# Kernel tuning notes

Measured on AMD Instinct MI355X. Metric: run time of the kernel, lower is better.

Reference implementation:

```python
import jax, jax.numpy as jnp
import numpy as np


def setup_inputs() -> dict:
    key = jax.random.key(0)
    k = jax.random.split(key, 8)
    B, S, D, H = 4, 4096, 1024, 4096
    x = jax.random.normal(k[0], (B, S, D), dtype=jnp.float32)
    # per-output-channel symmetric int8 weights in [-127, 127]
    w1_q = jax.random.randint(k[1], (H, D), -127, 128, dtype=jnp.int32)
    w2_q = jax.random.randint(k[2], (D, H), -127, 128, dtype=jnp.int32)
    # positive per-channel scales, roughly max|W|/127 for W ~ N(0, 0.02)
    s1 = jax.random.uniform(k[3], (H,), dtype=jnp.float32, minval=0.5, maxval=1.5) * (0.02 / 127.0)
    s2 = jax.random.uniform(k[4], (D,), dtype=jnp.float32, minval=0.5, maxval=1.5) * (0.02 / 127.0)
    b1 = jax.random.normal(k[5], (H,), dtype=jnp.float32) * 0.01
    b2 = jax.random.normal(k[6], (D,), dtype=jnp.float32) * 0.01
    return {"x": x, "w1_q": w1_q, "s1": s1, "b1": b1, "w2_q": w2_q, "s2": s2, "b2": b2}


def reference(x, w1_q, s1, b1, w2_q, s2, b2):
    # fc1: dequantize per-output-channel int8 weights, then GEMM + bias
    w1 = w1_q.astype(jnp.float32) * s1[:, None]          # [H, D]
    h = jnp.einsum('bsd,hd->bsh', x, w1) + b1            # [B, S, H]
    h = jax.nn.gelu(h, approximate=False)                # exact erf GELU (torch F.gelu default)
    # fc2: dequant + GEMM + bias
    w2 = w2_q.astype(jnp.float32) * s2[:, None]          # [D, H]
    y = jnp.einsum('bsh,dh->bsd', h, w2) + b2            # [B, S, D]
    return y
```

## Files before the change

kernel.cpp:

```cpp
#include <hip/hip_runtime.h>
#include <hip/hip_bf16.h>
#include <math.h>


typedef short bf16x8 __attribute__((ext_vector_type(8)));
typedef float f32x4 __attribute__((ext_vector_type(4)));

__device__ __forceinline__ unsigned short f2bf(float f) {
  unsigned int x = __float_as_uint(f);
  unsigned int r = (x + 0x7FFFu + ((x >> 16) & 1u)) >> 16;
  return (unsigned short)r;
}


__global__ void cvt_f32_bf16(const float* __restrict__ in,
                             unsigned short* __restrict__ out, int n4) {
  int i = blockIdx.x * blockDim.x + threadIdx.x;
  if (i >= n4) return;
  float4 v = reinterpret_cast<const float4*>(in)[i];
  ushort4 o;
  o.x = f2bf(v.x); o.y = f2bf(v.y); o.z = f2bf(v.z); o.w = f2bf(v.w);
  reinterpret_cast<ushort4*>(out)[i] = o;
}

__global__ void cvt_i32_bf16(const int* __restrict__ in,
                             unsigned short* __restrict__ out, int n4) {
  int i = blockIdx.x * blockDim.x + threadIdx.x;
  if (i >= n4) return;
  int4 v = reinterpret_cast<const int4*>(in)[i];
  ushort4 o;
  o.x = f2bf((float)v.x); o.y = f2bf((float)v.y);
  o.z = f2bf((float)v.z); o.w = f2bf((float)v.w);
  reinterpret_cast<ushort4*>(out)[i] = o;
}


#define BM 128
#define BN 128
#define BK 64

template <int EPI>
__global__ __launch_bounds__(256, 2) void gemm_bt(
    const unsigned short* __restrict__ A, const unsigned short* __restrict__ Bw,
    const float* __restrict__ scale, const float* __restrict__ bias,
    void* __restrict__ Cout, int M, int N, int K) {
  __shared__ unsigned short As[BM * BK];
  __shared__ unsigned short Bs[BN * BK];

  const int nwg = gridDim.x;
  const int orig = blockIdx.x;
  const int q = nwg >> 3, r = nwg & 7;
  const int xcd = orig & 7, idx = orig >> 3;
  const int swz =
      (xcd < r ? xcd * (q + 1) : r * (q + 1) + (xcd - r) * q) + idx;

  const int nBn = N / BN;
  const int bm = (swz / nBn) * BM;
  const int bn = (swz % nBn) * BN;

  const int tid = threadIdx.x;
  const int lane = tid & 63;
  const int wid = tid >> 6;
  const int wm = (wid >> 1) * 64;
  const int wn = (wid & 1) * 64;

  const int r0 = tid >> 3;
  const int c0 = (tid & 7) * 8;

  const unsigned short* aSrc = A + (size_t)(bm + r0) * K + c0;
  const unsigned short* bSrc = Bw + (size_t)(bn + r0) * K + c0;
  unsigned short* aDst = &As[r0 * BK + c0];
  unsigned short* bDst = &Bs[r0 * BK + c0];

  f32x4 acc[4][4];
#pragma unroll
  for (int i = 0; i < 4; ++i)
#pragma unroll
    for (int j = 0; j < 4; ++j) acc[i][j] = 0.0f;

  const int kIters = K / BK;
  for (int ks = 0; ks < kIters; ++ks) {
    const unsigned short* aS = aSrc + ks * BK;
    const unsigned short* bS = bSrc + ks * BK;
#pragma unroll
    for (int i = 0; i < 4; ++i) {
      __builtin_amdgcn_global_load_lds(
          (const __attribute__((address_space(1))) void*)(aS + (size_t)i * 32 * K),
          (__attribute__((address_space(3))) void*)(aDst + i * 32 * BK), 16, 0, 0);
    }
#pragma unroll
    for (int i = 0; i < 4; ++i) {
      __builtin_amdgcn_global_load_lds(
          (const __attribute__((address_space(1))) void*)(bS + (size_t)i * 32 * K),
          (__attribute__((address_space(3))) void*)(bDst + i * 32 * BK), 16, 0, 0);
    }
    __syncthreads();

#pragma unroll
    for (int kk = 0; kk < BK; kk += 32) {
      const int kOff = kk + (lane >> 4) * 8;
      bf16x8 a[4], b[4];
#pragma unroll
      for (int mi = 0; mi < 4; ++mi)
        a[mi] = *(const bf16x8*)&As[(wm + mi * 16 + (lane & 15)) * BK + kOff];
#pragma unroll
      for (int ni = 0; ni < 4; ++ni)
        b[ni] = *(const bf16x8*)&Bs[(wn + ni * 16 + (lane & 15)) * BK + kOff];
#pragma unroll
      for (int mi = 0; mi < 4; ++mi)
#pragma unroll
        for (int ni = 0; ni < 4; ++ni)
          acc[mi][ni] = __builtin_amdgcn_mfma_f32_16x16x32_bf16(
              a[mi], b[ni], acc[mi][ni], 0, 0, 0);
    }
    __syncthreads();
  }

  const int cr = (lane >> 4) * 4;
  const int cc = lane & 15;
#pragma unroll
  for (int ni = 0; ni < 4; ++ni) {
    const int gn = bn + wn + ni * 16 + cc;
    const float sv = scale[gn];
    const float bv = bias[gn];
#pragma unroll
    for (int mi = 0; mi < 4; ++mi) {
#pragma unroll
      for (int qq = 0; qq < 4; ++qq) {
        const size_t gm = (size_t)(bm + wm + mi * 16 + cr + qq);
        float v = acc[mi][ni][qq] * sv + bv;
        if (EPI == 0) {
          v = 0.5f * v * (1.0f + erff(v * 0.70710678118654752f));
          ((unsigned short*)Cout)[gm * N + gn] = f2bf(v);
        } else {
          ((float*)Cout)[gm * N + gn] = v;
        }
      }
    }
  }
}


extern "C" void kernel_launch(void* const* d_in, const int* in_sizes, int n_in,
                              void* d_out, int out_size, void* d_ws,
                              size_t ws_size, hipStream_t stream) {
  const float* x = (const float*)d_in[0];
  const int* w1q = (const int*)d_in[1];
  const float* s1 = (const float*)d_in[2];
  const float* b1 = (const float*)d_in[3];
  const int* w2q = (const int*)d_in[4];
  const float* s2 = (const float*)d_in[5];
  const float* b2 = (const float*)d_in[6];

  const int H = in_sizes[3];
  const int D = in_sizes[6];
  const int M = in_sizes[0] / D;

  char* ws = (char*)d_ws;
  unsigned short* xb = (unsigned short*)ws;  ws += (size_t)M * D * 2;
  unsigned short* w1b = (unsigned short*)ws; ws += (size_t)H * D * 2;
  unsigned short* w2b = (unsigned short*)ws; ws += (size_t)D * H * 2;
  unsigned short* hb = (unsigned short*)ws;  ws += (size_t)M * H * 2;

  {
    int n4 = M * D / 4;
    cvt_f32_bf16<<<(n4 + 255) / 256, 256, 0, stream>>>(x, xb, n4);
  }
  {
    int n4 = H * D / 4;
    cvt_i32_bf16<<<(n4 + 255) / 256, 256, 0, stream>>>(w1q, w1b, n4);
    cvt_i32_bf16<<<(n4 + 255) / 256, 256, 0, stream>>>(w2q, w2b, n4);
  }

  gemm_bt<0><<<(M / BM) * (H / BN), 256, 0, stream>>>(
      xb, w1b, s1, b1, (void*)hb, M, H, D);
  gemm_bt<1><<<(M / BM) * (D / BN), 256, 0, stream>>>(
      hb, w2b, s2, b2, d_out, M, D, H);
}
```

Before: 492.1 us.

## Rewrite GEMM as 256x256 tile, 8-wave, software-pipelined kernel with swizzled LDS

Replaces the 128x128 single-buffer GEMM with a 512-thread kernel that computes 256x256 output tiles. The K dimension is split into 32-wide slices staged into double-buffered LDS slots via global_load_lds, with a four-phase schedule that interleaves next-slice loads with MFMA work, raised priority around the MFMAs, and an XOR swizzle to avoid LDS bank conflicts. Conversion kernels now use grid-stride loops with 8-element vectors. This aims to overlap memory with compute and raise reuse per tile. In exchange, register pressure is higher with 32 accumulators per thread, and correctness depends on the hand-placed barriers and waitcnts.

```diff
diff --git a/kernel.cpp b/kernel.cpp
--- a/kernel.cpp
+++ b/kernel.cpp
@@ -5,6 +5,7 @@
 
 typedef short bf16x8 __attribute__((ext_vector_type(8)));
 typedef float f32x4 __attribute__((ext_vector_type(4)));
+typedef unsigned short u16x8 __attribute__((ext_vector_type(8)));
 
 __device__ __forceinline__ unsigned short f2bf(float f) {
   unsigned int x = __float_as_uint(f);
@@ -14,121 +15,170 @@
 
 
 __global__ void cvt_f32_bf16(const float* __restrict__ in,
-                             unsigned short* __restrict__ out, int n4) {
-  int i = blockIdx.x * blockDim.x + threadIdx.x;
-  if (i >= n4) return;
-  float4 v = reinterpret_cast<const float4*>(in)[i];
-  ushort4 o;
-  o.x = f2bf(v.x); o.y = f2bf(v.y); o.z = f2bf(v.z); o.w = f2bf(v.w);
-  reinterpret_cast<ushort4*>(out)[i] = o;
+                             unsigned short* __restrict__ out, int n8) {
+  const int stride = gridDim.x * blockDim.x;
+  for (int i = blockIdx.x * blockDim.x + threadIdx.x; i < n8; i += stride) {
+    const float4* p = (const float4*)(in + (size_t)i * 8);
+    float4 v0 = p[0], v1 = p[1];
+    u16x8 o;
+    o[0] = f2bf(v0.x); o[1] = f2bf(v0.y); o[2] = f2bf(v0.z); o[3] = f2bf(v0.w);
+    o[4] = f2bf(v1.x); o[5] = f2bf(v1.y); o[6] = f2bf(v1.z); o[7] = f2bf(v1.w);
+    *(u16x8*)(out + (size_t)i * 8) = o;
+  }
 }
 
 __global__ void cvt_i32_bf16(const int* __restrict__ in,
-                             unsigned short* __restrict__ out, int n4) {
-  int i = blockIdx.x * blockDim.x + threadIdx.x;
-  if (i >= n4) return;
-  int4 v = reinterpret_cast<const int4*>(in)[i];
-  ushort4 o;
-  o.x = f2bf((float)v.x); o.y = f2bf((float)v.y);
-  o.z = f2bf((float)v.z); o.w = f2bf((float)v.w);
-  reinterpret_cast<ushort4*>(out)[i] = o;
-}
-
-
-#define BM 128
-#define BN 128
-#define BK 64
+                             unsigned short* __restrict__ out, int n8) {
+  const int stride = gridDim.x * blockDim.x;
+  for (int i = blockIdx.x * blockDim.x + threadIdx.x; i < n8; i += stride) {
+    const int4* p = (const int4*)(in + (size_t)i * 8);
+    int4 v0 = p[0], v1 = p[1];
+    u16x8 o;
+    o[0] = f2bf((float)v0.x); o[1] = f2bf((float)v0.y);
+    o[2] = f2bf((float)v0.z); o[3] = f2bf((float)v0.w);
+    o[4] = f2bf((float)v1.x); o[5] = f2bf((float)v1.y);
+    o[6] = f2bf((float)v1.z); o[7] = f2bf((float)v1.w);
+    *(u16x8*)(out + (size_t)i * 8) = o;
+  }
+}
+
+
+#define NSLOT 8
+#define SLOTE 4096
+
+__device__ __forceinline__ void stage_half(
+    const unsigned short* __restrict__ gA, const unsigned short* __restrict__ gB,
+    int bm, int bn, int K, unsigned short* lds, int T, int w, int tid) {
+  const unsigned short* base =
+      (w >= 2) ? (gB + (size_t)(bn + (w & 1) * 128) * K)
+               : (gA + (size_t)(bm + (w & 1) * 128) * K);
+  base += T * 32;
+  unsigned short* slot = lds + ((((T & 1) << 2) | w) * SLOTE);
+  const int lr = tid >> 2;
+  const int colD = (tid & 3) * 8;
+  const int colS = colD ^ ((lr & 3) << 3);
+  __builtin_amdgcn_global_load_lds(
+      (const __attribute__((address_space(1))) void*)(base + (size_t)lr * K + colS),
+      (__attribute__((address_space(3))) void*)(slot + lr * 32 + colD), 16, 0, 0);
+}
+
+#define DS_A(asl, mi) \
+  (*(const bf16x8*)&lds[(asl) * SLOTE + ((mi) * 16 + l15) * 32 + c0])
+#define DS_B(bsl, ni) \
+  (*(const bf16x8*)&lds[(bsl) * SLOTE + (bRow + (ni) * 16 + l15) * 32 + c0])
+
+#define PHASE(p, sAslot, sBslot, STAGE, VM)                                    \
+  {                                                                            \
+    bf16x8 a0, a1;                                                             \
+    if ((p) == 0) {                                                            \
+      _Pragma("unroll") for (int ni = 0; ni < 4; ++ni) bfr[ni] =               \
+          DS_B(sBslot, ni);                                                    \
+    }                                                                          \
+    a0 = DS_A(sAslot, 2 * (p));                                                \
+    a1 = DS_A(sAslot, 2 * (p) + 1);                                            \
+    STAGE;                                                                     \
+    VM;                                                                        \
+    __builtin_amdgcn_s_barrier();                                              \
+    asm volatile("s_waitcnt lgkmcnt(0)" ::: "memory");                         \
+    __builtin_amdgcn_sched_barrier(0);                                         \
+    __builtin_amdgcn_s_setprio(1);                                             \
+    _Pragma("unroll") for (int ni = 0; ni < 4; ++ni) {                         \
+      acc[2 * (p)][ni] = __builtin_amdgcn_mfma_f32_16x16x32_bf16(              \
+          a0, bfr[ni], acc[2 * (p)][ni], 0, 0, 0);                             \
+      acc[2 * (p) + 1][ni] = __builtin_amdgcn_mfma_f32_16x16x32_bf16(          \
+          a1, bfr[ni], acc[2 * (p) + 1][ni], 0, 0, 0);                         \
+    }                                                                          \
+    __builtin_amdgcn_s_setprio(0);                                             \
+    __builtin_amdgcn_sched_barrier(0);                                         \
+    __builtin_amdgcn_s_barrier();                                              \
+  }
+
+#define VM2 asm volatile("s_waitcnt vmcnt(2)" ::: "memory")
+#define VM0 asm volatile("s_waitcnt vmcnt(0)" ::: "memory")
+#define STG(T_, w_) stage_half(A, Bw, bm, bn, K, lds, (T_), (w_), tid)
 
 template <int EPI>
-__global__ __launch_bounds__(256, 2) void gemm_bt(
+__global__ __launch_bounds__(512) void gemm8p(
     const unsigned short* __restrict__ A, const unsigned short* __restrict__ Bw,
     const float* __restrict__ scale, const float* __restrict__ bias,
     void* __restrict__ Cout, int M, int N, int K) {
-  __shared__ unsigned short As[BM * BK];
-  __shared__ unsigned short Bs[BN * BK];
+  __shared__ unsigned short lds[NSLOT * SLOTE];
 
   const int nwg = gridDim.x;
   const int orig = blockIdx.x;
-  const int q = nwg >> 3, r = nwg & 7;
-  const int xcd = orig & 7, idx = orig >> 3;
+  const int qx = nwg >> 3, rx = nwg & 7;
+  const int xcd = orig & 7, sidx = orig >> 3;
   const int swz =
-      (xcd < r ? xcd * (q + 1) : r * (q + 1) + (xcd - r) * q) + idx;
-
-  const int nBn = N / BN;
-  const int bm = (swz / nBn) * BM;
-  const int bn = (swz % nBn) * BN;
+      (xcd < rx ? xcd * (qx + 1) : rx * (qx + 1) + (xcd - rx) * qx) + sidx;
+
+  const int nBn = N / 256;
+  const int bm = (swz / nBn) * 256;
+  const int bn = (swz % nBn) * 256;
 
   const int tid = threadIdx.x;
   const int lane = tid & 63;
   const int wid = tid >> 6;
-  const int wm = (wid >> 1) * 64;
-  const int wn = (wid & 1) * 64;
-
-  const int r0 = tid >> 3;
-  const int c0 = (tid & 7) * 8;
-
-  const unsigned short* aSrc = A + (size_t)(bm + r0) * K + c0;
-  const unsigned short* bSrc = Bw + (size_t)(bn + r0) * K + c0;
-  unsigned short* aDst = &As[r0 * BK + c0];
-  unsigned short* bDst = &Bs[r0 * BK + c0];
-
-  f32x4 acc[4][4];
-#pragma unroll
-  for (int i = 0; i < 4; ++i)
+  const int wm = wid >> 2;
+  const int wn = wid & 3;
+
+  const int l15 = lane & 15;
+  const int c0 = (((lane >> 4) * 8)) ^ ((lane & 3) << 3);
+  const int bRow = (wn & 1) * 64;
+  const int bHalf = 2 + (wn >> 1);
+
+  f32x4 acc[8][4];
+#pragma unroll
+  for (int i = 0; i < 8; ++i)
 #pragma unroll
     for (int j = 0; j < 4; ++j) acc[i][j] = 0.0f;
 
-  const int kIters = K / BK;
-  for (int ks = 0; ks < kIters; ++ks) {
-    const unsigned short* aS = aSrc + ks * BK;
-    const unsigned short* bS = bSrc + ks * BK;
-#pragma unroll
-    for (int i = 0; i < 4; ++i) {
-      __builtin_amdgcn_global_load_lds(
-          (const __attribute__((address_space(1))) void*)(aS + (size_t)i * 32 * K),
-          (__attribute__((address_space(3))) void*)(aDst + i * 32 * BK), 16, 0, 0);
-    }
-#pragma unroll
-    for (int i = 0; i < 4; ++i) {
-      __builtin_amdgcn_global_load_lds(
-          (const __attribute__((address_space(1))) void*)(bS + (size_t)i * 32 * K),
-          (__attribute__((address_space(3))) void*)(bDst + i * 32 * BK), 16, 0, 0);
-    }
-    __syncthreads();
-
-#pragma unroll
-    for (int kk = 0; kk < BK; kk += 32) {
-      const int kOff = kk + (lane >> 4) * 8;
-      bf16x8 a[4], b[4];
-#pragma unroll
-      for (int mi = 0; mi < 4; ++mi)
-        a[mi] = *(const bf16x8*)&As[(wm + mi * 16 + (lane & 15)) * BK + kOff];
-#pragma unroll
-      for (int ni = 0; ni < 4; ++ni)
-        b[ni] = *(const bf16x8*)&Bs[(wn + ni * 16 + (lane & 15)) * BK + kOff];
-#pragma unroll
-      for (int mi = 0; mi < 4; ++mi)
-#pragma unroll
-        for (int ni = 0; ni < 4; ++ni)
-          acc[mi][ni] = __builtin_amdgcn_mfma_f32_16x16x32_bf16(
-              a[mi], b[ni], acc[mi][ni], 0, 0, 0);
-    }
-    __syncthreads();
-  }
-
-  const int cr = (lane >> 4) * 4;
-  const int cc = lane & 15;
+  bf16x8 bfr[4];
+
+  const int KT = K / 32;
+
+  STG(0, 2); STG(0, 3); STG(0, 0); STG(0, 1); STG(1, 2); STG(1, 3);
+  VM2;
+  __builtin_amdgcn_s_barrier();
+
+  for (int kt = 0; kt <= KT - 3; ++kt) {
+    const int sA = ((kt & 1) << 2) | wm;
+    const int sB = ((kt & 1) << 2) | bHalf;
+    PHASE(0, sA, sB, STG(kt + 1, 0), );
+    PHASE(1, sA, sB, STG(kt + 1, 1), );
+    PHASE(2, sA, sB, STG(kt + 2, 2), );
+    PHASE(3, sA, sB, STG(kt + 2, 3), VM2);
+  }
+  {
+    const int kt = KT - 2;
+    const int sA = ((kt & 1) << 2) | wm;
+    const int sB = ((kt & 1) << 2) | bHalf;
+    PHASE(0, sA, sB, STG(kt + 1, 0), );
+    PHASE(1, sA, sB, STG(kt + 1, 1), );
+    PHASE(2, sA, sB, , );
+    PHASE(3, sA, sB, , VM0);
+  }
+  {
+    const int kt = KT - 1;
+    const int sA = ((kt & 1) << 2) | wm;
+    const int sB = ((kt & 1) << 2) | bHalf;
+    PHASE(0, sA, sB, , );
+    PHASE(1, sA, sB, , );
+    PHASE(2, sA, sB, , );
+    PHASE(3, sA, sB, , );
+  }
+
+  const int crow = (lane >> 4) * 4;
 #pragma unroll
   for (int ni = 0; ni < 4; ++ni) {
-    const int gn = bn + wn + ni * 16 + cc;
+    const int gn = bn + wn * 64 + ni * 16 + l15;
     const float sv = scale[gn];
     const float bv = bias[gn];
 #pragma unroll
-    for (int mi = 0; mi < 4; ++mi) {
-#pragma unroll
-      for (int qq = 0; qq < 4; ++qq) {
-        const size_t gm = (size_t)(bm + wm + mi * 16 + cr + qq);
-        float v = acc[mi][ni][qq] * sv + bv;
+    for (int mi = 0; mi < 8; ++mi) {
+#pragma unroll
+      for (int qv = 0; qv < 4; ++qv) {
+        const size_t gm = (size_t)(bm + wm * 128 + mi * 16 + crow + qv);
+        float v = acc[mi][ni][qv] * sv + bv;
         if (EPI == 0) {
           v = 0.5f * v * (1.0f + erff(v * 0.70710678118654752f));
           ((unsigned short*)Cout)[gm * N + gn] = f2bf(v);
@@ -162,18 +212,12 @@
   unsigned short* w2b = (unsigned short*)ws; ws += (size_t)D * H * 2;
   unsigned short* hb = (unsigned short*)ws;  ws += (size_t)M * H * 2;
 
-  {
-    int n4 = M * D / 4;
-    cvt_f32_bf16<<<(n4 + 255) / 256, 256, 0, stream>>>(x, xb, n4);
-  }
-  {
-    int n4 = H * D / 4;
-    cvt_i32_bf16<<<(n4 + 255) / 256, 256, 0, stream>>>(w1q, w1b, n4);
-    cvt_i32_bf16<<<(n4 + 255) / 256, 256, 0, stream>>>(w2q, w2b, n4);
-  }
-
-  gemm_bt<0><<<(M / BM) * (H / BN), 256, 0, stream>>>(
+  cvt_f32_bf16<<<2048, 256, 0, stream>>>(x, xb, M * D / 8);
+  cvt_i32_bf16<<<2048, 256, 0, stream>>>(w1q, w1b, H * D / 8);
+  cvt_i32_bf16<<<2048, 256, 0, stream>>>(w2q, w2b, D * H / 8);
+
+  gemm8p<0><<<(M / 256) * (H / 256), 512, 0, stream>>>(
       xb, w1b, s1, b1, (void*)hb, M, H, D);
-  gemm_bt<1><<<(M / BM) * (D / BN), 256, 0, stream>>>(
+  gemm8p<1><<<(M / 256) * (D / 256), 512, 0, stream>>>(
       hb, w2b, s2, b2, d_out, M, D, H);
 }
```

New measurement: 462.9 us. 5.9% less time.
